# Performance work log

Hardware: AMD Instinct MI355X
Metric: run time of the kernel (lower is better)

Reference implementation:

```python
import jax, jax.numpy as jnp
import numpy as np
import math

B, S, H = 2, 4096, 512
NUM_HEADS = 8
HEAD_DIM = H // NUM_HEADS
RECENCY_DECAY = 0.9


def setup_inputs() -> dict:
    key = jax.random.key(0)
    k1, k2, k3 = jax.random.split(key, 3)
    scale = 1.0 / math.sqrt(H)
    x = jax.random.normal(k1, (B, S, H), dtype=jnp.float32)
    w_qkv = jax.random.normal(k2, (3 * H, H), dtype=jnp.float32) * scale
    w_out = jax.random.normal(k3, (H, H), dtype=jnp.float32) * scale
    b_out = jnp.zeros((H,), dtype=jnp.float32)
    return {"x": x, "w_qkv": w_qkv, "w_out": w_out, "b_out": b_out}


def reference(x, w_qkv, w_out, b_out):
    batch, seq_len, hidden = x.shape
    nh, hd = NUM_HEADS, HEAD_DIM
    # qkv projection (no bias): torch Linear computes x @ W.T
    qkv = jnp.einsum('bsh,oh->bso', x, w_qkv)
    qkv = qkv.reshape(batch, seq_len, 3, nh, hd)
    q, k, v = jnp.transpose(qkv, (2, 0, 3, 1, 4))  # each [B, nh, S, hd]
    attn = jnp.einsum('bhqd,bhkd->bhqk', q, k) / math.sqrt(hd)
    # recency bias: positions[i, j] = j - i; bias = (j-i)*log(decay) for j<=i else 0
    pos = jnp.arange(seq_len)[None, :] - jnp.arange(seq_len)[:, None]
    bias = jnp.where(pos <= 0, pos.astype(jnp.float32) * math.log(RECENCY_DECAY),
                     jnp.zeros((), dtype=jnp.float32))
    attn = jax.nn.softmax(attn + bias[None, None, :, :], axis=-1)
    out = jnp.einsum('bhqk,bhkd->bqhd', attn, v).reshape(batch, seq_len, hidden)
    return jnp.einsum('bsh,oh->bso', out, w_out) + b_out
```

## Files before the change

### kernel.cpp

```cpp
#include <hip/hip_runtime.h>
#include <hip/hip_bf16.h>
#include <hip/hip_fp16.h>
#include <stdint.h>

#define B_   2
#define S_   4096
#define H_   512
#define NH_  8
#define HD_  64
#define M_   (B_*S_)
#define LOG2D (-0.15200309344504997f)
#define SC2   (0.18033688011112042f)

#define NFULL        4
#define NCHUNK       8

typedef __attribute__((ext_vector_type(8))) short bf16x8_t;
typedef __attribute__((ext_vector_type(4))) float f32x4_t;

__device__ __forceinline__ void gl_lds16(const __hip_bfloat16* g, __hip_bfloat16* l) {
  __builtin_amdgcn_global_load_lds(
      (__attribute__((address_space(1))) void*)(g),
      (__attribute__((address_space(3))) void*)(l),
      16, 0, 0);
}

__global__ __launch_bounds__(256)
void cast3_kernel(const float* __restrict__ x, const float* __restrict__ wq,
                  const float* __restrict__ wo,
                  __hip_bfloat16* __restrict__ xb, __hip_bfloat16* __restrict__ wqb,
                  __hip_bfloat16* __restrict__ wob) {
  const int N0 = M_ * H_;
  const int N1 = 3 * H_ * H_;
  int i4 = (blockIdx.x * blockDim.x + threadIdx.x) * 4;
  const float* src; __hip_bfloat16* dst; int off;
  if (i4 < N0)           { src = x;  dst = xb;  off = i4; }
  else if (i4 < N0 + N1) { src = wq; dst = wqb; off = i4 - N0; }
  else                   { src = wo; dst = wob; off = i4 - N0 - N1; }
  float4 v = *(const float4*)(src + off);
  ushort4 o;
  __hip_bfloat16 h;
  h = __float2bfloat16(v.x); o.x = *(unsigned short*)&h;
  h = __float2bfloat16(v.y); o.y = *(unsigned short*)&h;
  h = __float2bfloat16(v.z); o.z = *(unsigned short*)&h;
  h = __float2bfloat16(v.w); o.w = *(unsigned short*)&h;
  *(ushort4*)((unsigned short*)dst + off) = o;
}

template<int EPI>
__global__ __launch_bounds__(256)
void gemm_bt(const __hip_bfloat16* __restrict__ A,
             const __hip_bfloat16* __restrict__ Bw,
             int K,
             __hip_bfloat16* __restrict__ qb,
             __hip_bfloat16* __restrict__ kb,
             __hip_bfloat16* __restrict__ vtb,
             float* __restrict__ outp,
             const float* __restrict__ bias) {
  __shared__ alignas(16) __hip_bfloat16 sA[128*64];
  __shared__ alignas(16) __hip_bfloat16 sB[128*64];
  const int tid  = threadIdx.x;
  const int wave = tid >> 6, lane = tid & 63;
  const int quad = lane >> 4, l15 = lane & 15;
  const int wr = (wave >> 1) * 64, wc = (wave & 1) * 64;

  const int nbx  = gridDim.x;
  const int flat = blockIdx.y * nbx + blockIdx.x;
  const int xcd  = flat & 7, sq = flat >> 3;
  const int rows_per_xcd = gridDim.y >> 3;
  const int by = xcd * rows_per_xcd + sq / nbx;
  const int bx = sq % nbx;
  const int m0 = by * 128, n0 = bx * 128;

  const int sub  = lane >> 3;
  const int plog = (lane & 7) ^ sub;

  f32x4_t acc[4][4] = {};

  for (int kt = 0; kt < K; kt += 64) {
    __syncthreads();
    #pragma unroll
    for (int cc = 0; cc < 4; cc++) {
      int c   = wave * 4 + cc;
      int row = c * 8 + sub;
      gl_lds16(A  + (size_t)(m0 + row) * K + kt + plog * 8, sA + c * 512);
      gl_lds16(Bw + (size_t)(n0 + row) * K + kt + plog * 8, sB + c * 512);
    }
    __syncthreads();
    #pragma unroll
    for (int kh = 0; kh < 2; kh++) {
      bf16x8_t af[4], bfr[4];
      #pragma unroll
      for (int x = 0; x < 4; x++) {
        int row = wr + x * 16 + l15;
        int pos = kh * 4 + quad;
        af[x] = *(const bf16x8_t*)(sA + row * 64 + ((pos ^ (row & 7)) << 3));
      }
      #pragma unroll
      for (int y = 0; y < 4; y++) {
        int row = wc + y * 16 + l15;
        int pos = kh * 4 + quad;
        bfr[y] = *(const bf16x8_t*)(sB + row * 64 + ((pos ^ (row & 7)) << 3));
      }
      #pragma unroll
      for (int x = 0; x < 4; x++)
        #pragma unroll
        for (int y = 0; y < 4; y++)
          acc[x][y] = __builtin_amdgcn_mfma_f32_16x16x32_bf16(af[x], bfr[y], acc[x][y], 0, 0, 0);
    }
  }

  if (EPI == 0 && (n0 >> 9) == 2) {
    #pragma unroll
    for (int x = 0; x < 4; x++) {
      int gr = m0 + wr + x * 16 + quad * 4;
      int bb = gr >> 12, sb = gr & 4095;
      #pragma unroll
      for (int y = 0; y < 4; y++) {
        int rem = (n0 - 1024) + wc + y * 16 + l15;
        int h = rem >> 6, d = rem & 63;
        ushort4 o; __hip_bfloat16 hv;
        hv = __float2bfloat16(acc[x][y][0]); o.x = *(unsigned short*)&hv;
        hv = __float2bfloat16(acc[x][y][1]); o.y = *(unsigned short*)&hv;
        hv = __float2bfloat16(acc[x][y][2]); o.z = *(unsigned short*)&hv;
        hv = __float2bfloat16(acc[x][y][3]); o.w = *(unsigned short*)&hv;
        *(ushort4*)(vtb + ((size_t)(bb * NH_ + h) * HD_ + d) * S_ + sb) = o;
      }
    }
  } else {
    #pragma unroll
    for (int x = 0; x < 4; x++) {
      #pragma unroll
      for (int y = 0; y < 4; y++) {
        #pragma unroll
        for (int r = 0; r < 4; r++) {
          int gr = m0 + wr + x*16 + quad*4 + r;
          int gc = n0 + wc + y*16 + l15;
          float v = acc[x][y][r];
          if (EPI == 0) {
            int bb = gr >> 12, s = gr & 4095;
            int t  = gc >> 9,  rem = gc & 511;
            int h  = rem >> 6, d = rem & 63;
            __hip_bfloat16 hv = __float2bfloat16(v);
            int bh = bb * NH_ + h;
            if (t == 0) qb[((size_t)bh * S_ + s) * HD_ + d] = hv;
            else        kb[((size_t)bh * S_ + s) * HD_ + d] = hv;
          } else {
            outp[(size_t)gr * H_ + gc] = v + bias[gc];
          }
        }
      }
    }
  }
}

__device__ __forceinline__ void stage_kv(const __hip_bfloat16* __restrict__ kb,
                                         const __hip_bfloat16* __restrict__ vtb,
                                         int bh, int j0,
                                         __hip_bfloat16* dK, __hip_bfloat16* dV,
                                         int wave, int lane, int sub, int plog) {
  if (wave < 2) {
    #pragma unroll
    for (int cc = 0; cc < 4; cc++) {
      int c = wave * 4 + cc;
      gl_lds16(kb + ((size_t)bh * S_ + j0 + c * 8 + sub) * HD_ + plog * 8, dK + c * 512);
    }
  } else {
    #pragma unroll
    for (int cc = 0; cc < 4; cc++) {
      int c = (wave - 2) * 4 + cc;
      gl_lds16(vtb + ((size_t)bh * HD_ + c * 8 + sub) * S_ + j0 + plog * 8, dV + c * 512);
    }
  }
}

__global__ __launch_bounds__(256)
void attn_kernel(const __hip_bfloat16* __restrict__ qb,
                 const __hip_bfloat16* __restrict__ kb,
                 const __hip_bfloat16* __restrict__ vtb,
                 __hip_bfloat16* __restrict__ ob,
                 __half* __restrict__ pO,
                 float* __restrict__ pl) {
  __shared__ alignas(16) __hip_bfloat16 sK[2][64*64];
  __shared__ alignas(16) __hip_bfloat16 sV[2][64*64];
  __shared__ alignas(16) __hip_bfloat16 sP[4][16*64];

  const int tid  = threadIdx.x;
  const int wave = tid >> 6, lane = tid & 63;
  const int quad = lane >> 4, l15 = lane & 15;

  const int flat = blockIdx.x;
  const int xcd  = flat & 7;
  const int idx  = flat >> 3;
  const int b1   = idx / 92;
  const int w    = idx % 92;
  const int bh   = xcd + (b1 << 3);

  int q0, jt0, niter, chunk = 0;
  bool direct;
  if (w < 60) { q0 = 256 + w * 64; jt0 = 0; niter = 4; direct = true; }
  else { int t = w - 60; chunk = t & 7; q0 = (t >> 3) * 64; jt0 = chunk * 8; niter = 8; direct = false; }

  const __hip_bfloat16* qrow = qb + ((size_t)bh * S_ + q0 + wave * 16 + l15) * HD_;
  bf16x8_t aQ0 = *(const bf16x8_t*)(qrow + quad * 8);
  bf16x8_t aQ1 = *(const bf16x8_t*)(qrow + 32 + quad * 8);

  f32x4_t accO[4] = {};
  float l_r[4], negM2[4];
  const int row_i = q0 + wave * 16 + quad * 4;
  #pragma unroll
  for (int r = 0; r < 4; r++) {
    l_r[r] = 0.f;
    negM2[r] = -(17.312340f - LOG2D * (float)(row_i + r));
  }

  const int sub  = lane >> 3;
  const int plog = (lane & 7) ^ sub;
  __hip_bfloat16* sPw = &sP[wave][0];

  stage_kv(kb, vtb, bh, jt0 * 64, &sK[0][0], &sV[0][0], wave, lane, sub, plog);

  for (int it = 0; it < niter; ++it) {
    const int cur = it & 1;
    __syncthreads();
    if (it < niter - 1)
      stage_kv(kb, vtb, bh, (jt0 + it + 1) * 64,
               &sK[1 - cur][0], &sV[1 - cur][0], wave, lane, sub, plog);
    const __hip_bfloat16* cK = &sK[cur][0];
    const __hip_bfloat16* cV = &sV[cur][0];
    const int j0 = (jt0 + it) * 64;

    f32x4_t sfr[4];
    __builtin_amdgcn_s_setprio(1);
    #pragma unroll
    for (int ni = 0; ni < 4; ni++) {
      int row = ni * 16 + l15;
      f32x4_t a = {};
      bf16x8_t b0 = *(const bf16x8_t*)(cK + row * 64 + ((quad       ^ (row & 7)) << 3));
      bf16x8_t b1v = *(const bf16x8_t*)(cK + row * 64 + (((quad + 4) ^ (row & 7)) << 3));
      a = __builtin_amdgcn_mfma_f32_16x16x32_bf16(aQ0, b0, a, 0, 0, 0);
      a = __builtin_amdgcn_mfma_f32_16x16x32_bf16(aQ1, b1v, a, 0, 0, 0);
      sfr[ni] = a;
    }
    __builtin_amdgcn_s_setprio(0);

    #pragma unroll
    for (int r = 0; r < 4; r++) {
      const float d0 = (float)(j0 + l15 - (row_i + r));
      const int row = quad * 4 + r;
      float psum = 0.f;
      #pragma unroll
      for (int ni = 0; ni < 4; ni++) {
        float dij = d0 + (float)(ni * 16);
        float arg = fmaf(fminf(dij, 0.f), LOG2D, fmaf(sfr[ni][r], SC2, negM2[r]));
        float p = __builtin_amdgcn_exp2f(arg);
        psum += p;
        int col = ni * 16 + l15;
        sPw[row * 64 + (((col >> 3) ^ (row & 7)) << 3) + (col & 7)] = __float2bfloat16(p);
      }
      l_r[r] += psum;
    }
    __builtin_amdgcn_sched_barrier(0);
    __builtin_amdgcn_s_waitcnt(0xC07F);
    __builtin_amdgcn_sched_barrier(0);

    bf16x8_t aP0 = *(const bf16x8_t*)(sPw + l15 * 64 + ((quad       ^ (l15 & 7)) << 3));
    bf16x8_t aP1 = *(const bf16x8_t*)(sPw + l15 * 64 + (((quad + 4) ^ (l15 & 7)) << 3));
    __builtin_amdgcn_s_setprio(1);
    #pragma unroll
    for (int nd = 0; nd < 4; nd++) {
      int row = nd * 16 + l15;
      bf16x8_t b0 = *(const bf16x8_t*)(cV + row * 64 + ((quad       ^ (row & 7)) << 3));
      bf16x8_t b1v = *(const bf16x8_t*)(cV + row * 64 + (((quad + 4) ^ (row & 7)) << 3));
      accO[nd] = __builtin_amdgcn_mfma_f32_16x16x32_bf16(aP0, b0, accO[nd], 0, 0, 0);
      accO[nd] = __builtin_amdgcn_mfma_f32_16x16x32_bf16(aP1, b1v, accO[nd], 0, 0, 0);
    }
    __builtin_amdgcn_s_setprio(0);
    __builtin_amdgcn_sched_barrier(0);
  }

  #pragma unroll
  for (int r = 0; r < 4; r++) {
    float l = l_r[r];
    #pragma unroll
    for (int msk = 1; msk < 16; msk <<= 1) l += __shfl_xor(l, msk, 64);
    l_r[r] = l;
  }

  if (direct) {
    const int b = bh >> 3, h = bh & 7;
    #pragma unroll
    for (int r = 0; r < 4; r++) {
      float invr = 1.0f / l_r[r];
      #pragma unroll
      for (int nd = 0; nd < 4; nd++) {
        int srow = q0 + wave * 16 + quad * 4 + r;
        int col  = h * HD_ + nd * 16 + l15;
        ob[((size_t)b * S_ + srow) * H_ + col] = __float2bfloat16(accO[nd][r] * invr);
      }
    }
  } else {
    const int qt = q0 >> 6;
    size_t base = ((size_t)bh * NFULL + qt) * NCHUNK + chunk;
    __half* po = pO + base * 4096;
    #pragma unroll
    for (int nd = 0; nd < 4; nd++)
      #pragma unroll
      for (int r = 0; r < 4; r++)
        po[(wave*16 + quad*4 + r) * 64 + nd*16 + l15] = __float2half(accO[nd][r]);
    if (l15 == 0) {
      #pragma unroll
      for (int r = 0; r < 4; r++)
        pl[base * 64 + wave*16 + quad*4 + r] = l_r[r];
    }
  }
}

__global__ __launch_bounds__(256)
void combine_kernel(const __half* __restrict__ pO,
                    const float* __restrict__ pl,
                    __hip_bfloat16* __restrict__ ob) {
  const int f  = blockIdx.x;
  const int bh = blockIdx.y;
  const int tid = threadIdx.x;
  const int rr = tid >> 2, cg = (tid & 3) * 16;
  const size_t base0 = ((size_t)bh * NFULL + f) * NCHUNK;

  float L = 0.f;
  #pragma unroll
  for (int c = 0; c < NCHUNK; c++) L += pl[(base0 + c) * 64 + rr];
  const float inv = 1.0f / L;

  float o[16];
  #pragma unroll
  for (int k = 0; k < 16; k++) o[k] = 0.f;
  #pragma unroll
  for (int c = 0; c < NCHUNK; c++) {
    const __half* src = pO + (base0 + c) * 4096 + rr * 64 + cg;
    #pragma unroll
    for (int k = 0; k < 16; k++) o[k] += __half2float(src[k]);
  }
  const int b = bh >> 3, h = bh & 7, s = f * 64 + rr;
  __hip_bfloat16* dst = ob + ((size_t)b * S_ + s) * H_ + h * HD_ + cg;
  #pragma unroll
  for (int k = 0; k < 16; k++) dst[k] = __float2bfloat16(o[k] * inv);
}

extern "C" void kernel_launch(void* const* d_in, const int* in_sizes, int n_in,
                              void* d_out, int out_size, void* d_ws, size_t ws_size,
                              hipStream_t stream) {
  const float* x     = (const float*)d_in[0];
  const float* w_qkv = (const float*)d_in[1];
  const float* w_out = (const float*)d_in[2];
  const float* b_out = (const float*)d_in[3];
  float* out = (float*)d_out;

  char* ws = (char*)d_ws;
  __hip_bfloat16* xb  = (__hip_bfloat16*)(ws);
  __hip_bfloat16* wqb = (__hip_bfloat16*)(ws + (8u  << 20));
  __hip_bfloat16* wob = (__hip_bfloat16*)(ws + (10u << 20));
  __hip_bfloat16* qb  = (__hip_bfloat16*)(ws + (11u << 20));
  __hip_bfloat16* kb  = (__hip_bfloat16*)(ws + (19u << 20));
  __hip_bfloat16* vtb = (__hip_bfloat16*)(ws + (27u << 20));
  __half*         pO  = (__half*)(ws + (36u << 20));
  float*          pl  = (float*)(ws + (41u << 20));
  __hip_bfloat16* ab  = xb;

  cast3_kernel<<<dim3(5120), dim3(256), 0, stream>>>(x, w_qkv, w_out, xb, wqb, wob);
  gemm_bt<0><<<dim3(12, 64), dim3(256), 0, stream>>>(xb, wqb, H_, qb, kb, vtb, nullptr, nullptr);
  attn_kernel<<<dim3(1472), dim3(256), 0, stream>>>(qb, kb, vtb, ab, pO, pl);
  combine_kernel<<<dim3(NFULL, B_ * NH_), dim3(256), 0, stream>>>(pO, pl, ab);
  gemm_bt<1><<<dim3(4, 64), dim3(256), 0, stream>>>(ab, wob, H_, nullptr, nullptr, nullptr, out, b_out);
}
```

Baseline: 136.4 us.

## Fuse split-KV combine into attention kernel via atomic last-block reduction

Removes the separate combine kernel launch. Each split-chunk block of the attention kernel now increments a per-(head, query-tile) counter after writing its partial output, and the last arriving block performs the reduction and writes the final bf16 output. Counters are zeroed in the cast kernel. This saves one launch and its dependency gap, but adds fences, atomics and a serialized tail reduction inside the attention kernel.

```diff
diff --git a/kernel.cpp b/kernel.cpp
--- a/kernel.cpp
+++ b/kernel.cpp
@@ -29,7 +29,9 @@
 void cast3_kernel(const float* __restrict__ x, const float* __restrict__ wq,
                   const float* __restrict__ wo,
                   __hip_bfloat16* __restrict__ xb, __hip_bfloat16* __restrict__ wqb,
-                  __hip_bfloat16* __restrict__ wob) {
+                  __hip_bfloat16* __restrict__ wob, int* __restrict__ cnt) {
+  if (blockIdx.x == 0 && threadIdx.x < NFULL * B_ * NH_)
+    cnt[threadIdx.x] = 0;
   const int N0 = M_ * H_;
   const int N1 = 3 * H_ * H_;
   int i4 = (blockIdx.x * blockDim.x + threadIdx.x) * 4;
@@ -180,10 +182,12 @@
                  const __hip_bfloat16* __restrict__ vtb,
                  __hip_bfloat16* __restrict__ ob,
                  __half* __restrict__ pO,
-                 float* __restrict__ pl) {
+                 float* __restrict__ pl,
+                 int* __restrict__ cnt) {
   __shared__ alignas(16) __hip_bfloat16 sK[2][64*64];
   __shared__ alignas(16) __hip_bfloat16 sV[2][64*64];
   __shared__ alignas(16) __hip_bfloat16 sP[4][16*64];
+  __shared__ int s_old;
 
   const int tid  = threadIdx.x;
   const int wave = tid >> 6, lane = tid & 63;
@@ -301,7 +305,7 @@
     }
   } else {
     const int qt = q0 >> 6;
-    size_t base = ((size_t)bh * NFULL + qt) * NCHUNK + chunk;
+    const size_t base = ((size_t)bh * NFULL + qt) * NCHUNK + chunk;
     __half* po = pO + base * 4096;
     #pragma unroll
     for (int nd = 0; nd < 4; nd++)
@@ -313,37 +317,35 @@
       for (int r = 0; r < 4; r++)
         pl[base * 64 + wave*16 + quad*4 + r] = l_r[r];
     }
-  }
-}
-
-__global__ __launch_bounds__(256)
-void combine_kernel(const __half* __restrict__ pO,
-                    const float* __restrict__ pl,
-                    __hip_bfloat16* __restrict__ ob) {
-  const int f  = blockIdx.x;
-  const int bh = blockIdx.y;
-  const int tid = threadIdx.x;
-  const int rr = tid >> 2, cg = (tid & 3) * 16;
-  const size_t base0 = ((size_t)bh * NFULL + f) * NCHUNK;
-
-  float L = 0.f;
-  #pragma unroll
-  for (int c = 0; c < NCHUNK; c++) L += pl[(base0 + c) * 64 + rr];
-  const float inv = 1.0f / L;
-
-  float o[16];
-  #pragma unroll
-  for (int k = 0; k < 16; k++) o[k] = 0.f;
-  #pragma unroll
-  for (int c = 0; c < NCHUNK; c++) {
-    const __half* src = pO + (base0 + c) * 4096 + rr * 64 + cg;
-    #pragma unroll
-    for (int k = 0; k < 16; k++) o[k] += __half2float(src[k]);
-  }
-  const int b = bh >> 3, h = bh & 7, s = f * 64 + rr;
-  __hip_bfloat16* dst = ob + ((size_t)b * S_ + s) * H_ + h * HD_ + cg;
-  #pragma unroll
-  for (int k = 0; k < 16; k++) dst[k] = __float2bfloat16(o[k] * inv);
+
+    __syncthreads();
+    __threadfence();
+    __syncthreads();
+    if (tid == 0) s_old = atomicAdd(&cnt[bh * NFULL + qt], 1);
+    __syncthreads();
+    if (s_old == NCHUNK - 1) {
+      __threadfence();
+      const int rr = tid >> 2, cg = (tid & 3) * 16;
+      const size_t base0 = ((size_t)bh * NFULL + qt) * NCHUNK;
+      float L = 0.f;
+      #pragma unroll
+      for (int c = 0; c < NCHUNK; c++) L += pl[(base0 + c) * 64 + rr];
+      const float inv = 1.0f / L;
+      float o[16];
+      #pragma unroll
+      for (int k = 0; k < 16; k++) o[k] = 0.f;
+      #pragma unroll
+      for (int c = 0; c < NCHUNK; c++) {
+        const __half* src = pO + (base0 + c) * 4096 + rr * 64 + cg;
+        #pragma unroll
+        for (int k = 0; k < 16; k++) o[k] += __half2float(src[k]);
+      }
+      const int b = bh >> 3, h = bh & 7, s = qt * 64 + rr;
+      __hip_bfloat16* dst = ob + ((size_t)b * S_ + s) * H_ + h * HD_ + cg;
+      #pragma unroll
+      for (int k = 0; k < 16; k++) dst[k] = __float2bfloat16(o[k] * inv);
+    }
+  }
 }
 
 extern "C" void kernel_launch(void* const* d_in, const int* in_sizes, int n_in,
@@ -364,11 +366,11 @@
   __hip_bfloat16* vtb = (__hip_bfloat16*)(ws + (27u << 20));
   __half*         pO  = (__half*)(ws + (36u << 20));
   float*          pl  = (float*)(ws + (41u << 20));
+  int*            cnt = (int*)(ws + (42u << 20));
   __hip_bfloat16* ab  = xb;
 
-  cast3_kernel<<<dim3(5120), dim3(256), 0, stream>>>(x, w_qkv, w_out, xb, wqb, wob);
+  cast3_kernel<<<dim3(5120), dim3(256), 0, stream>>>(x, w_qkv, w_out, xb, wqb, wob, cnt);
   gemm_bt<0><<<dim3(12, 64), dim3(256), 0, stream>>>(xb, wqb, H_, qb, kb, vtb, nullptr, nullptr);
-  attn_kernel<<<dim3(1472), dim3(256), 0, stream>>>(qb, kb, vtb, ab, pO, pl);
-  combine_kernel<<<dim3(NFULL, B_ * NH_), dim3(256), 0, stream>>>(pO, pl, ab);
+  attn_kernel<<<dim3(1472), dim3(256), 0, stream>>>(qb, kb, vtb, ab, pO, pl, cnt);
   gemm_bt<1><<<dim3(4, 64), dim3(256), 0, stream>>>(ab, wob, H_, nullptr, nullptr, nullptr, out, b_out);
 }
```

Measured after the change: 196.0 us. 1.44x slower.
